# Performance work log

Measured on AMD Instinct MI355X. Metric: run time of the kernel, lower is better.

The kernel has to match this reference:

```python
import jax, jax.numpy as jnp
import numpy as np
from jax import lax

B, NQ, C = 2, 1024, 2048
H, DH = 16, 128
G, CD = 4, 512          # off_grps, off_dim = C // G
LR, HR = 24, 72         # low-res grid side, high-res grid side
INTER = 64
K = LR * LR             # sampled K/V tokens (grid_size == lr_size)


def setup_inputs() -> dict:
    key = jax.random.key(0)
    ks = jax.random.split(key, 16)
    s = 0.02
    d = {}
    d['hidden_states'] = jax.random.normal(ks[0], (B, NQ, C), jnp.float32)
    d['image_hd'] = jax.random.normal(ks[1], (B, HR * HR, C), jnp.float32)
    d['wq'] = jax.random.normal(ks[2], (C, C), jnp.float32) * s
    d['wk'] = jax.random.normal(ks[3], (C, C), jnp.float32) * s
    d['wv'] = jax.random.normal(ks[4], (C, C), jnp.float32) * s
    d['wo'] = jax.random.normal(ks[5], (C, C), jnp.float32) * s
    d['conv_dw_w'] = jax.random.normal(ks[6], (CD, 1, 3, 3), jnp.float32) * s
    d['ln1_w'] = jnp.ones((CD,), jnp.float32)
    d['ln1_b'] = jnp.zeros((CD,), jnp.float32)
    d['conv_lr_proj_w'] = jax.random.normal(ks[7], (INTER, CD), jnp.float32) * s
    d['proj_int_w'] = jax.random.normal(ks[8], (INTER, CD), jnp.float32) * s
    d['proj_int_b'] = jnp.zeros((INTER,), jnp.float32)
    d['ln2_w'] = jnp.ones((INTER,), jnp.float32)
    d['ln2_b'] = jnp.zeros((INTER,), jnp.float32)
    d['conv_off_w'] = jax.random.normal(ks[9], (2, INTER), jnp.float32) * s
    d['k_hd_w'] = jax.random.normal(ks[10], (C, C), jnp.float32) * s
    d['k_hd_b'] = jnp.zeros((C,), jnp.float32)
    d['v_hd_w'] = jax.random.normal(ks[11], (C, C), jnp.float32) * s
    d['v_hd_b'] = jnp.zeros((C,), jnp.float32)
    return d


def _ln_channels(x, w, b, eps=1e-5):
    # LayerNorm2d: normalize over channel axis of [N, C, H, W]
    mu = jnp.mean(x, axis=1, keepdims=True)
    var = jnp.var(x, axis=1, keepdims=True)
    xn = (x - mu) * lax.rsqrt(var + eps)
    return xn * w[None, :, None, None] + b[None, :, None, None]


def _tokens_to_grid(x, S):
    # [B, S*S, C] -> [B*G, CD, S, S]  (group channels like einops '(b) (h w) (g c) -> (b g) c h w')
    return x.reshape(B, S, S, G, CD).transpose(0, 3, 4, 1, 2).reshape(B * G, CD, S, S)


def _bilinear_sample(img, grid):
    # img [N, C, Hh, Wh]; grid [N, K, 2] (x, y) normalized to [-1, 1], align_corners=True
    N, Cc, Hh, Wh = img.shape
    x = (grid[..., 0] + 1.0) * 0.5 * (Wh - 1)
    y = (grid[..., 1] + 1.0) * 0.5 * (Hh - 1)
    x0f, y0f = jnp.floor(x), jnp.floor(y)
    wx = (x - x0f)[:, None, :]
    wy = (y - y0f)[:, None, :]
    x0 = jnp.clip(x0f.astype(jnp.int32), 0, Wh - 1)
    x1 = jnp.clip(x0 + 1, 0, Wh - 1)
    y0 = jnp.clip(y0f.astype(jnp.int32), 0, Hh - 1)
    y1 = jnp.clip(y0 + 1, 0, Hh - 1)
    imgf = img.reshape(N, Cc, Hh * Wh)
    gather = jax.vmap(lambda im, ix: im[:, ix])  # ([C,HW],[K]) -> [C,K]
    v00 = gather(imgf, y0 * Wh + x0)
    v01 = gather(imgf, y0 * Wh + x1)
    v10 = gather(imgf, y1 * Wh + x0)
    v11 = gather(imgf, y1 * Wh + x1)
    return (v00 * (1 - wx) * (1 - wy) + v01 * wx * (1 - wy)
            + v10 * (1 - wx) * wy + v11 * wx * wy)  # [N, C, K]


def _ref_grid():
    # normalized reference points as in _grid_generate (centers / (S-1) * 2 - 1)
    yy = (jnp.linspace(0.5, LR - 0.5, LR) / (LR - 1.0)) * 2.0 - 1.0
    xx = (jnp.linspace(0.5, LR - 0.5, LR) / (LR - 1.0)) * 2.0 - 1.0
    gy, gx = jnp.meshgrid(yy, xx, indexing='ij')
    return jnp.stack([gx, gy], axis=-1).reshape(K, 2)  # (x, y)


def reference(hidden_states, image_hd, wq, wk, wv, wo, conv_dw_w, ln1_w, ln1_b,
              conv_lr_proj_w, proj_int_w, proj_int_b, ln2_w, ln2_b, conv_off_w,
              k_hd_w, k_hd_b, v_hd_w, v_hd_b):
    # ---- QKV on the full sequence ----
    q = hidden_states @ wq.T
    k_txt = hidden_states @ wk.T
    v_txt = hidden_states @ wv.T

    # ---- offset network on LR image tokens (first LR*LR tokens) ----
    lr = _tokens_to_grid(hidden_states[:, :K, :], LR)          # [B*G, CD, LR, LR]
    x = lax.conv_general_dilated(lr, conv_dw_w, (1, 1), 'SAME',
                                 feature_group_count=CD,
                                 dimension_numbers=('NCHW', 'OIHW', 'NCHW'))
    x = jax.nn.silu(x)
    x = _ln_channels(x, ln1_w, ln1_b)
    x = jnp.einsum('nchw,oc->nohw', x, conv_lr_proj_w)          # 1x1 conv -> [B*G, INTER, LR, LR]
    # intention gate from spatially pooled group features
    pooled = jnp.mean(lr, axis=(2, 3))                          # [B*G, CD]
    gate = jax.nn.sigmoid(pooled @ proj_int_w.T + proj_int_b)   # [B*G, INTER]
    x = x * gate[:, :, None, None]
    x = _ln_channels(x, ln2_w, ln2_b)
    off = jnp.einsum('nchw,oc->nohw', x, conv_off_w)            # [B*G, 2, LR, LR]
    off = off.transpose(0, 2, 3, 1).reshape(B * G, K, 2)        # (x, y)
    pos = jnp.tanh(_ref_grid()[None] + off)                     # sampling locs in [-1, 1]

    # ---- deformable gather from HD features ----
    hd = _tokens_to_grid(image_hd, HR)                          # [B*G, CD, HR, HR]
    samp = _bilinear_sample(hd, pos)                            # [B*G, CD, K]
    samp = samp.reshape(B, G, CD, K).transpose(0, 3, 1, 2).reshape(B, K, C)
    k_hd = samp @ k_hd_w.T + k_hd_b
    v_hd = samp @ v_hd_w.T + v_hd_b

    # ---- attention: causal over text tokens, HD tokens fully visible ----
    k_all = jnp.concatenate([k_txt, k_hd], axis=1)              # [B, NQ+K, C]
    v_all = jnp.concatenate([v_txt, v_hd], axis=1)
    qh = q.reshape(B, NQ, H, DH).transpose(0, 2, 1, 3)
    kh = k_all.reshape(B, NQ + K, H, DH).transpose(0, 2, 1, 3)
    vh = v_all.reshape(B, NQ + K, H, DH).transpose(0, 2, 1, 3)
    scores = jnp.einsum('bhqd,bhkd->bhqk', qh, kh) / jnp.sqrt(jnp.float32(DH))
    col = jnp.arange(NQ + K)
    row = jnp.arange(NQ)
    allow = (col[None, :] >= NQ) | (col[None, :] <= row[:, None])
    scores = jnp.where(allow[None, None], scores, jnp.float32(-1e9))
    attn = jax.nn.softmax(scores, axis=-1)
    out = jnp.einsum('bhqk,bhkd->bhqd', attn, vh)
    out = out.transpose(0, 2, 1, 3).reshape(B, NQ, C)
    return out @ wo.T
```

## Files before the change

kernel.cpp:

```cpp
#include <hip/hip_runtime.h>

typedef unsigned short u16;
typedef unsigned int u32;
typedef __attribute__((ext_vector_type(8))) short bf8;
typedef __attribute__((ext_vector_type(4))) float f4;
typedef __attribute__((ext_vector_type(4))) unsigned short us4;

constexpr int B = 2;
constexpr int NQ = 1024;
constexpr int C = 2048;
constexpr int DH = 128;
constexpr int G = 4;
constexpr int CD = 512;
constexpr int LR = 24;
constexpr int HR = 72;
constexpr int INTER = 64;
constexpr int K = LR * LR;
constexpr int NKV = NQ + K;

#define MFMA16(a, b, c) __builtin_amdgcn_mfma_f32_16x16x32_bf16(a, b, c, 0, 0, 0)
#define GLDS(g, l)                                                         \
  __builtin_amdgcn_global_load_lds(                                        \
      (const __attribute__((address_space(1))) void*)(g),                  \
      (__attribute__((address_space(3))) void*)(l), 16, 0, 0)
#define SB()                               \
  do {                                     \
    __builtin_amdgcn_sched_barrier(0);     \
    __builtin_amdgcn_s_barrier();          \
    __builtin_amdgcn_sched_barrier(0);     \
  } while (0)
#define WVM(n)                                              \
  do {                                                      \
    asm volatile("s_waitcnt vmcnt(" #n ")" ::: "memory");   \
    __builtin_amdgcn_sched_barrier(0);                      \
  } while (0)

__device__ __forceinline__ u16 f2bf1(float f) {
  u32 u = __float_as_uint(f);
  u32 r = (u + 0x7fffu + ((u >> 16) & 1u)) >> 16;
  return (u16)r;
}

__global__ __launch_bounds__(256) void f2bf_k8v(
    const float* __restrict__ s0, const float* __restrict__ s1,
    const float* __restrict__ s2, const float* __restrict__ s3,
    const float* __restrict__ s4, const float* __restrict__ s5,
    const float* __restrict__ s6, const float* __restrict__ plrw,
    u16* __restrict__ d0, u16* __restrict__ d1, u16* __restrict__ d2,
    u16* __restrict__ d3, u16* __restrict__ d4, u16* __restrict__ d5,
    u16* __restrict__ d6, float* __restrict__ wt) {
  __shared__ u16 L[64 * 68];
  const int y = blockIdx.y;
  const int t = threadIdx.x;
  if (y == 7) {
    if (blockIdx.x >= 128) return;
    const int idx = blockIdx.x * 256 + t;
    wt[idx] = plrw[(idx & 63) * 512 + (idx >> 6)];
    return;
  }
  const float* s;
  u16* d;
  switch (y) {
    case 0: s = s0; d = d0; break;
    case 1: s = s1; d = d1; break;
    case 2: s = s2; d = d2; break;
    case 3: s = s3; d = d3; break;
    case 4: s = s4; d = d4; break;
    case 5: s = s5; d = d5; break;
    default: s = s6; d = d6; break;
  }
  const int pc = blockIdx.x;
  const int mb = pc >> 5, kb = pc & 31;
  const int rin = t >> 2, c0 = (t & 3) * 16;
  const float* src = s + (size_t)(mb * 64 + rin) * 2048 + kb * 64 + c0;
#pragma unroll
  for (int j = 0; j < 16; j += 4) {
    float4 v = *(const float4*)(src + j);
    L[rin * 68 + c0 + j] = f2bf1(v.x);
    L[rin * 68 + c0 + j + 1] = f2bf1(v.y);
    L[rin * 68 + c0 + j + 2] = f2bf1(v.z);
    L[rin * 68 + c0 + j + 3] = f2bf1(v.w);
  }
  __syncthreads();
  u16* dst = d + (size_t)pc * 4096 + t * 16;
#pragma unroll
  for (int gg = 0; gg < 2; ++gg) {
    const int g = t * 2 + gg;
    const int rh = g & 15, ks2 = (g >> 4) & 3, kc = (g >> 6) & 1, fr = g >> 7;
    const int row = fr * 16 + rh, cc = kc * 32 + ks2 * 8;
    us4 o0, o1;
    o0.x = L[row * 68 + cc];     o0.y = L[row * 68 + cc + 1];
    o0.z = L[row * 68 + cc + 2]; o0.w = L[row * 68 + cc + 3];
    o1.x = L[row * 68 + cc + 4]; o1.y = L[row * 68 + cc + 5];
    o1.z = L[row * 68 + cc + 6]; o1.w = L[row * 68 + cc + 7];
    *(us4*)(dst + gg * 8) = o0;
    *(us4*)(dst + gg * 8 + 4) = o1;
  }
}

__global__ __launch_bounds__(256) void dwpool16(const float* __restrict__ hs,
                                                const float* __restrict__ cdw,
                                                float* __restrict__ x1,
                                                float* __restrict__ pooled) {
  __shared__ float SH[16 * 577];
  const int bidx = blockIdx.x;
  const int n = bidx >> 5, cg = bidx & 31;
  const int b = n >> 2, g = n & 3;
  const int c0 = cg * 16;
  const int t = threadIdx.x;
  {
    const int c = t & 15, pr = t >> 4;
    const float* src = hs + (size_t)b * 1024 * 2048 + g * 512 + c0 + c;
#pragma unroll 4
    for (int j = 0; j < 36; ++j) {
      const int p = j * 16 + pr;
      SH[c * 577 + p] = src[(size_t)p * 2048];
    }
  }
  __syncthreads();
  {
    const int c = t >> 4, seg = t & 15;
    float s = 0.f;
    for (int i = 0; i < 36; ++i) s += SH[c * 577 + seg * 36 + i];
    s += __shfl_xor(s, 1);
    s += __shfl_xor(s, 2);
    s += __shfl_xor(s, 4);
    s += __shfl_xor(s, 8);
    if (seg == 0) pooled[n * 512 + c0 + c] = s * (1.f / 576.f);
  }
  const size_t base_out = (size_t)(n * 512 + c0) * 576;
  for (int j = 0; j < 36; ++j) {
    const int idx = j * 256 + t;
    const int c = idx / 576, p = idx - c * 576;
    const int yy0 = p / 24, xx0 = p - yy0 * 24;
    const float* wp = cdw + (c0 + c) * 9;
    float s = 0.f;
#pragma unroll
    for (int dy = -1; dy <= 1; ++dy)
#pragma unroll
      for (int dx = -1; dx <= 1; ++dx) {
        const int yy = yy0 + dy, xx = xx0 + dx;
        if (yy < 0 || yy >= 24 || xx < 0 || xx >= 24) continue;
        s += SH[c * 577 + yy * 24 + xx] * wp[(dy + 1) * 3 + dx + 1];
      }
    x1[base_out + idx] = s / (1.f + expf(-s));
  }
}

__global__ __launch_bounds__(512, 2) void gemm_queue(
    const u16* __restrict__ Ast, const u16* __restrict__ Wq,
    const u16* __restrict__ Wk, const u16* __restrict__ Wv,
    const u16* __restrict__ sampst, const u16* __restrict__ khwst,
    const u16* __restrict__ vhwst, const float* __restrict__ khb,
    const float* __restrict__ vhb, u16* __restrict__ outq,
    u16* __restrict__ kg, u16* __restrict__ vg, u32* __restrict__ qctr) {
  __shared__ u16 As[2][4][4096];
  __shared__ u16 Bs[2][4][4096];
  __shared__ int s_item;
  const int tid = threadIdx.x, lane = tid & 63, w = tid >> 6;
  const int ks = lane >> 4, r = lane & 15;

  while (true) {
    __syncthreads();
    if (tid == 0) s_item = (int)atomicAdd(qctr, 1u);
    __syncthreads();
    const int item = s_item;
    if (item >= 480) break;

    if (item < 192) {
      const int wm = w >> 2, wn = w & 3;
      const int swz = (item & 7) * 24 + (item >> 3);
      const int mt = swz / 24, nt = swz % 24;
      const u16* Wst = (nt < 8) ? Wq : (nt < 16) ? Wk : Wv;
      const int nb0 = (nt & 7) * 4;
      const int mb0 = mt * 4;

#define ST_A03(bi, kt)                                                        \
  do {                                                                        \
    GLDS(Ast + ((size_t)(mb0 + 0) * 32 + (kt)) * 4096 + tid * 8,              \
         &As[bi][0][tid * 8]);                                                \
    GLDS(Ast + ((size_t)(mb0 + 2) * 32 + (kt)) * 4096 + tid * 8,              \
         &As[bi][2][tid * 8]);                                                \
  } while (0)
#define ST_A47(bi, kt)                                                        \
  do {                                                                        \
    GLDS(Ast + ((size_t)(mb0 + 1) * 32 + (kt)) * 4096 + tid * 8,              \
         &As[bi][1][tid * 8]);                                                \
    GLDS(Ast + ((size_t)(mb0 + 3) * 32 + (kt)) * 4096 + tid * 8,              \
         &As[bi][3][tid * 8]);                                                \
  } while (0)
#define ST_B01(bi, kt)                                                        \
  do {                                                                        \
    GLDS(Wst + ((size_t)(nb0 + 0) * 32 + (kt)) * 4096 + tid * 8,              \
         &Bs[bi][0][tid * 8]);                                                \
    GLDS(Wst + ((size_t)(nb0 + 1) * 32 + (kt)) * 4096 + tid * 8,              \
         &Bs[bi][1][tid * 8]);                                                \
  } while (0)
#define ST_B23(bi, kt)                                                        \
  do {                                                                        \
    GLDS(Wst + ((size_t)(nb0 + 2) * 32 + (kt)) * 4096 + tid * 8,              \
         &Bs[bi][2][tid * 8]);                                                \
    GLDS(Wst + ((size_t)(nb0 + 3) * 32 + (kt)) * 4096 + tid * 8,              \
         &Bs[bi][3][tid * 8]);                                                \
  } while (0)
#define RD_A(dst, bi, half, kc)                                               \
  _Pragma("unroll") for (int i2 = 0; i2 < 4; ++i2) dst[i2] =                  \
      *(const bf8*)(&As[bi][wm * 2 + (half)]                                  \
                       [((i2 * 2 + (kc)) * 4 + ks) * 128 + r * 8]);
#define RD_B(dst, bi, kc)                                                     \
  _Pragma("unroll") for (int j2 = 0; j2 < 4; ++j2) dst[j2] =                  \
      *(const bf8*)(&Bs[bi][wn][((j2 * 2 + (kc)) * 4 + ks) * 128 + r * 8]);
#define MM(ACC, AF, BF)                                                       \
  do {                                                                        \
    __builtin_amdgcn_s_setprio(1);                                            \
    _Pragma("unroll") for (int i3 = 0; i3 < 4; ++i3)                          \
        _Pragma("unroll") for (int j3 = 0; j3 < 4; ++j3) ACC[i3][j3] =        \
            MFMA16(AF[i3], BF[j3], ACC[i3][j3]);                              \
    __builtin_amdgcn_s_setprio(0);                                            \
  } while (0)

      f4 accA[4][4], accB[4][4];
#pragma unroll
      for (int i = 0; i < 4; ++i)
#pragma unroll
        for (int j = 0; j < 4; ++j) {
          accA[i][j] = f4{0.f, 0.f, 0.f, 0.f};
          accB[i][j] = f4{0.f, 0.f, 0.f, 0.f};
        }
      bf8 af[4], b0[4], b1[4];

      ST_A03(0, 0); ST_B01(0, 0); ST_B23(0, 0); ST_A47(0, 0);
      ST_A03(1, 1); ST_B01(1, 1);
      WVM(6);
      SB();

      for (int t = 0; t < 32; ++t) {
        const int buf = t & 1;
        RD_A(af, buf, 0, 0);
        RD_B(b0, buf, 0);
        if (t + 1 < 32) ST_B23(buf ^ 1, t + 1);
        SB();
        MM(accA, af, b0);
        SB();
        RD_A(af, buf, 0, 1);
        RD_B(b1, buf, 1);
        if (t + 1 < 32) ST_A47(buf ^ 1, t + 1);
        SB();
        MM(accA, af, b1);
        if (t + 1 < 32) { WVM(8); } else { WVM(0); }
        SB();
        RD_A(af, buf, 1, 0);
        if (t + 2 < 32) ST_A03(buf, t + 2);
        SB();
        MM(accB, af, b0);
        SB();
        RD_A(af, buf, 1, 1);
        if (t + 2 < 32) ST_B01(buf, t + 2);
        SB();
        MM(accB, af, b1);
        if (t + 2 < 32) { WVM(6); } else if (t + 1 < 32) { WVM(2); }
        SB();
      }

#define EPI(ACC, HALF)                                                        \
  _Pragma("unroll") for (int i = 0; i < 4; ++i)                               \
      _Pragma("unroll") for (int j = 0; j < 4; ++j)                           \
          _Pragma("unroll") for (int rr = 0; rr < 4; ++rr) {                  \
    const int m = mt * 256 + wm * 128 + (HALF)*64 + i * 16 + ks * 4 + rr;     \
    const int n = nt * 256 + wn * 64 + j * 16 + r;                            \
    const float v = ACC[i][j][rr];                                            \
    const int sel = n >> 11, nn = n & 2047, hh = nn >> 7, dd = nn & 127;      \
    const int bb = m >> 10, qq = m & 1023;                                    \
    const u16 bv = f2bf1(v);                                                  \
    if (sel == 0) {                                                           \
      outq[(size_t)m * 2048 + nn] = bv;                                       \
    } else if (sel == 1) {                                                    \
      kg[(((size_t)(bb * 16 + hh) * 50 + (qq >> 5)) * 16 + (dd >> 3)) * 256 + \
         (qq & 31) * 8 + (dd & 7)] = bv;                                      \
    } else {                                                                  \
      vg[((size_t)(bb * 16 + hh) * 200 + (qq >> 3)) * 1024 + dd * 8 +         \
         (qq & 7)] = bv;                                                      \
    }                                                                         \
  }
      EPI(accA, 0)
      EPI(accB, 1)
#undef EPI
    } else {
      u16* A3 = &As[0][0][0];
      u16* B3 = &Bs[0][0][0];
      const int htile = item - 192;
      const bool is_v = (htile >= 144);
      const int hb = is_v ? (htile - 144) : htile;
      const int mt = hb / 16, nt = hb % 16;
      const int ma0 = mt * 2, nb0 = nt * 2;
      const int wr = w >> 2, wc = w & 3;
      const u16* Wsrc = is_v ? vhwst : khwst;

#define HDS1(bi, kt)                                                          \
  do {                                                                        \
    const int kb_ = (kt) >> 1, kc_ = (kt) & 1;                                \
    GLDS(sampst + ((size_t)(ma0 + (w >> 2)) * 32 + kb_) * 4096 +              \
             (w & 3) * 1024 + kc_ * 512 + lane * 8,                           \
         &A3[(bi)*4096 + w * 512 + lane * 8]);                                \
    GLDS(Wsrc + ((size_t)(nb0 + (w >> 2)) * 32 + kb_) * 4096 +                \
             (w & 3) * 1024 + kc_ * 512 + lane * 8,                           \
         &B3[(bi)*4096 + w * 512 + lane * 8]);                                \
  } while (0)

      f4 acc[4][2];
#pragma unroll
      for (int i = 0; i < 4; ++i)
#pragma unroll
        for (int j = 0; j < 2; ++j) acc[i][j] = f4{0.f, 0.f, 0.f, 0.f};

      HDS1(0, 0);
      HDS1(1, 1);
      int rd = 0;
      for (int kt = 0; kt < 64; ++kt) {
        SB();
        if (kt + 2 < 64) {
          const int wb = (rd + 2 >= 3) ? rd - 1 : rd + 2;
          HDS1(wb, kt + 2);
          WVM(4);
        } else if (kt + 1 < 64) {
          WVM(2);
        } else {
          WVM(0);
        }
        SB();
        bf8 af2[4], bw[2];
#pragma unroll
        for (int i = 0; i < 4; ++i)
          af2[i] = *(const bf8*)(&A3[rd * 4096 + (wr * 4 + i) * 512 +
                                     ks * 128 + r * 8]);
#pragma unroll
        for (int j = 0; j < 2; ++j)
          bw[j] = *(const bf8*)(&B3[rd * 4096 + (wc * 2 + j) * 512 +
                                    ks * 128 + r * 8]);
        __builtin_amdgcn_s_setprio(1);
#pragma unroll
        for (int i = 0; i < 4; ++i)
#pragma unroll
          for (int j = 0; j < 2; ++j)
            acc[i][j] = MFMA16(af2[i], bw[j], acc[i][j]);
        __builtin_amdgcn_s_setprio(0);
        rd = (rd + 1 >= 3) ? 0 : rd + 1;
      }
#undef HDS1
      const int rbase = ks * 4;
      const float* bias = is_v ? vhb : khb;
#pragma unroll
      for (int i = 0; i < 4; ++i)
#pragma unroll
        for (int j = 0; j < 2; ++j) {
          const int nn = nt * 128 + (wc * 2 + j) * 16 + r;
          const int hh = nn >> 7, dd = nn & 127;
#pragma unroll
          for (int rr = 0; rr < 4; ++rr) {
            const int m = mt * 128 + wr * 64 + i * 16 + rbase + rr;
            const int bb = m / 576;
            const int kv = 1024 + (m - bb * 576);
            const u16 bv = f2bf1(acc[i][j][rr] + bias[nn]);
            if (!is_v) {
              kg[(((size_t)(bb * 16 + hh) * 50 + (kv >> 5)) * 16 + (dd >> 3)) *
                     256 +
                 (kv & 31) * 8 + (dd & 7)] = bv;
            } else {
              vg[((size_t)(bb * 16 + hh) * 200 + (kv >> 3)) * 1024 + dd * 8 +
                 (kv & 7)] = bv;
            }
          }
        }
    }
  }
}

__global__ __launch_bounds__(256) void gemm_out3(const u16* __restrict__ Ast,
                                                 const u16* __restrict__ W0,
                                                 float* __restrict__ outf) {
  __shared__ u16 As[3][4096];
  __shared__ u16 Bs[3][4096];
  const int tid = threadIdx.x, lane = tid & 63, w = tid >> 6;
  const int wr = w >> 1, wc = w & 1;
  const int ksl = lane >> 4, rl = lane & 15;
  const int xcd = blockIdx.x & 7, idx = blockIdx.x >> 3;
  const int mt = (xcd >> 2) * 8 + idx / 4;
  const int nt = (xcd & 3) * 4 + idx % 4;
  const u16* Wp = W0;
  const int ma0 = mt * 2;
  const int nb0 = nt * 2;

#define GST2(dstArr, srcBase, tb0, kt)                                     \
  do {                                                                     \
    const int kb_ = (kt) >> 1, kc_ = (kt) & 1;                             \
    _Pragma("unroll") for (int r2 = 0; r2 < 2; ++r2) {                     \
      const int run = r2 * 4 + w;                                          \
      GLDS(srcBase + ((size_t)((tb0) + (run >> 2)) * 32 + kb_) * 4096 +    \
               (run & 3) * 1024 + kc_ * 512 + lane * 8,                    \
           &dstArr[run * 512 + lane * 8]);                                 \
    }                                                                      \
  } while (0)

  f4 acc[4][4];
#pragma unroll
  for (int i = 0; i < 4; ++i)
#pragma unroll
    for (int j = 0; j < 4; ++j) acc[i][j] = f4{0.f, 0.f, 0.f, 0.f};

  GST2(As[0], Ast, ma0, 0);
  GST2(Bs[0], Wp, nb0, 0);
  GST2(As[1], Ast, ma0, 1);
  GST2(Bs[1], Wp, nb0, 1);
  int rd = 0;
  for (int kt = 0; kt < 64; ++kt) {
    SB();
    if (kt + 2 < 64) {
      const int wb = (rd + 2 >= 3) ? rd - 1 : rd + 2;
      GST2(As[wb], Ast, ma0, kt + 2);
      GST2(Bs[wb], Wp, nb0, kt + 2);
      WVM(8);
    } else if (kt + 1 < 64) {
      WVM(4);
    } else {
      WVM(0);
    }
    SB();
    bf8 af[4], bw[4];
#pragma unroll
    for (int i = 0; i < 4; ++i)
      af[i] = *(const bf8*)(&As[rd][(wr * 4 + i) * 512 + ksl * 128 + rl * 8]);
#pragma unroll
    for (int j = 0; j < 4; ++j)
      bw[j] = *(const bf8*)(&Bs[rd][(wc * 4 + j) * 512 + ksl * 128 + rl * 8]);
    __builtin_amdgcn_s_setprio(1);
#pragma unroll
    for (int i = 0; i < 4; ++i)
#pragma unroll
      for (int j = 0; j < 4; ++j)
        acc[i][j] = MFMA16(af[i], bw[j], acc[i][j]);
    __builtin_amdgcn_s_setprio(0);
    rd = (rd + 1 >= 3) ? 0 : rd + 1;
  }
#undef GST2

  const int rbase = ksl * 4;
#pragma unroll
  for (int i = 0; i < 4; ++i)
#pragma unroll
    for (int j = 0; j < 4; ++j) {
      const int n = nt * 128 + wc * 64 + j * 16 + rl;
#pragma unroll
      for (int rr = 0; rr < 4; ++rr) {
        const int m = mt * 128 + wr * 64 + i * 16 + rbase + rr;
        outf[(size_t)m * 2048 + n] = acc[i][j][rr];
      }
    }
}

__global__ __launch_bounds__(256) void lnproj_gate(
    const float* __restrict__ x1, const float* __restrict__ ln1w,
    const float* __restrict__ ln1b, const float* __restrict__ wt,
    const float* __restrict__ pooled, const float* __restrict__ piw,
    const float* __restrict__ pib, float* __restrict__ x2,
    float* __restrict__ gate) {
  __shared__ float Xs[512][68];
  __shared__ float rs[4][64], rss[4][64];
  const int bidx = blockIdx.x;
  const int t = threadIdx.x;
  if (bidx >= 72) {
    const int idx = (bidx - 72) * 256 + t;
    const int n = idx >> 6, o = idx & 63;
    const float* pb = pooled + n * 512;
    const float* wb = piw + o * 512;
    float s = pib[o];
    for (int c = 0; c < 512; ++c) s += pb[c] * wb[c];
    gate[idx] = 1.f / (1.f + expf(-s));
    return;
  }
  const int n = bidx / 9, pc = bidx % 9;
  const int p0 = pc * 64;
  {
    const int pl = t & 63, c4 = t >> 6;
    const float* src = x1 + (size_t)n * 512 * 576 + p0 + pl;
#pragma unroll 4
    for (int j = 0; j < 128; ++j) {
      const int c = j * 4 + c4;
      Xs[c][pl] = src[(size_t)c * 576];
    }
  }
  __syncthreads();
  {
    const int pl = t & 63, q = t >> 6;
    float s = 0.f, ss = 0.f;
    for (int c = q * 128; c < q * 128 + 128; ++c) {
      const float v = Xs[c][pl];
      s += v;
      ss += v * v;
    }
    rs[q][pl] = s;
    rss[q][pl] = ss;
    __syncthreads();
    const float S = rs[0][pl] + rs[1][pl] + rs[2][pl] + rs[3][pl];
    const float SS = rss[0][pl] + rss[1][pl] + rss[2][pl] + rss[3][pl];
    const float mean = S * (1.f / 512.f);
    const float inv = rsqrtf(SS * (1.f / 512.f) - mean * mean + 1e-5f);
    for (int c = q * 128; c < q * 128 + 128; ++c)
      Xs[c][pl] = (Xs[c][pl] - mean) * inv * ln1w[c] + ln1b[c];
  }
  __syncthreads();
  {
    const int o4 = (t & 15) * 4, pl0 = (t >> 4) * 4;
    float acc[4][4] = {};
    for (int c = 0; c < 512; ++c) {
      const f4 xv = *(const f4*)(&Xs[c][pl0]);
      const f4 wv = *(const f4*)(&wt[c * 64 + o4]);
#pragma unroll
      for (int i = 0; i < 4; ++i)
#pragma unroll
        for (int j = 0; j < 4; ++j) acc[i][j] += wv[i] * xv[j];
    }
#pragma unroll
    for (int i = 0; i < 4; ++i) {
      f4 ov;
      ov[0] = acc[i][0]; ov[1] = acc[i][1];
      ov[2] = acc[i][2]; ov[3] = acc[i][3];
      *(f4*)(&x2[(size_t)(n * 64 + o4 + i) * 576 + p0 + pl0]) = ov;
    }
  }
}

__global__ __launch_bounds__(256) void pos_sample(
    const float* __restrict__ x2, const float* __restrict__ gate,
    const float* __restrict__ ln2w, const float* __restrict__ ln2b,
    const float* __restrict__ offw, const float* __restrict__ img,
    u16* __restrict__ sampst) {
  const int bk = blockIdx.x;
  const int b = bk / K, k = bk % K;
  __shared__ int s_idx[G][4];
  __shared__ float s_w[G][4];
  const int t = threadIdx.x;
  const int g = t >> 6, lane = t & 63;
  {
    const int n = b * G + g;
    float v = x2[((size_t)n * INTER + lane) * K + k] * gate[n * INTER + lane];
    float s = v, ss = v * v;
    for (int o = 32; o; o >>= 1) {
      s += __shfl_xor(s, o);
      ss += __shfl_xor(ss, o);
    }
    const float mean = s * (1.f / INTER);
    const float var = ss * (1.f / INTER) - mean * mean;
    const float xn = (v - mean) * rsqrtf(var + 1e-5f) * ln2w[lane] + ln2b[lane];
    float ox = xn * offw[lane];
    float oy = xn * offw[INTER + lane];
    for (int o = 32; o; o >>= 1) {
      ox += __shfl_xor(ox, o);
      oy += __shfl_xor(oy, o);
    }
    if (lane == 0) {
      const int yi = k / LR, xi = k % LR;
      const float rx = (xi + 0.5f) / 23.f * 2.f - 1.f;
      const float ry = (yi + 0.5f) / 23.f * 2.f - 1.f;
      const float px = tanhf(rx + ox), py = tanhf(ry + oy);
      const float x = (px + 1.f) * 0.5f * (HR - 1);
      const float y = (py + 1.f) * 0.5f * (HR - 1);
      const float x0f = floorf(x), y0f = floorf(y);
      const float wx = x - x0f, wy = y - y0f;
      const int x0 = min(max((int)x0f, 0), HR - 1);
      const int x1 = min(x0 + 1, HR - 1);
      const int y0 = min(max((int)y0f, 0), HR - 1);
      const int y1 = min(y0 + 1, HR - 1);
      s_idx[g][0] = y0 * HR + x0;
      s_idx[g][1] = y0 * HR + x1;
      s_idx[g][2] = y1 * HR + x0;
      s_idx[g][3] = y1 * HR + x1;
      s_w[g][0] = (1.f - wx) * (1.f - wy);
      s_w[g][1] = wx * (1.f - wy);
      s_w[g][2] = (1.f - wx) * wy;
      s_w[g][3] = wx * wy;
    }
  }
  __syncthreads();
  const int m = b * 576 + k;
  const int mb = m >> 6, fr = (m >> 4) & 3, r = m & 15;
  const int ch0 = t * 8;
  const int gg = ch0 >> 9;
  const float* ib = img + (size_t)b * HR * HR * C + ch0;
  float v[8];
#pragma unroll
  for (int j = 0; j < 8; ++j) v[j] = 0.f;
#pragma unroll
  for (int q = 0; q < 4; ++q) {
    const float wq_ = s_w[gg][q];
    const float* p = ib + (size_t)s_idx[gg][q] * C;
    const float4 a = *(const float4*)p;
    const float4 c = *(const float4*)(p + 4);
    v[0] += wq_ * a.x; v[1] += wq_ * a.y; v[2] += wq_ * a.z; v[3] += wq_ * a.w;
    v[4] += wq_ * c.x; v[5] += wq_ * c.y; v[6] += wq_ * c.z; v[7] += wq_ * c.w;
  }
  const int kb = ch0 >> 6, kc = (ch0 >> 5) & 1, ks3 = (ch0 >> 3) & 3;
  u16* dst = sampst + ((size_t)(mb * 32 + kb)) * 4096 +
             (((fr * 2 + kc) * 4 + ks3) * 16 + r) * 8;
  us4 o0, o1;
  o0.x = f2bf1(v[0]); o0.y = f2bf1(v[1]); o0.z = f2bf1(v[2]); o0.w = f2bf1(v[3]);
  o1.x = f2bf1(v[4]); o1.y = f2bf1(v[5]); o1.z = f2bf1(v[6]); o1.w = f2bf1(v[7]);
  *(us4*)dst = o0;
  *(us4*)(dst + 4) = o1;
}

__global__ __launch_bounds__(256) void attn_u64(
    const u16* __restrict__ qb, const u16* __restrict__ kg,
    const u16* __restrict__ vg, u16* __restrict__ aob_st) {
  const int i = blockIdx.x;
  const int pair = i & 255, half = i >> 8;
  const int bh = pair & 31;
  const int q8 = pair >> 5;
  const int qblk = half ? (15 - q8) : q8;
  const int b = bh >> 4, h = bh & 15;
  const int q0 = qblk * 64;
  const int tid = threadIdx.x, lane = tid & 63, w = tid >> 6;
  const int qw = q0 + w * 16;
  const int col = lane & 15, kpart = lane >> 4, rbase = kpart * 4;
  __shared__ u16 Ks[2][8192];
  __shared__ u16 Vs[2][8192];
  __shared__ u16 Pl[4][16 * 72];
  bf8 qf[4];
  {
    const u16* qp =
        qb + (size_t)(b * 1024 + qw + col) * 2048 + h * 128 + kpart * 8;
#pragma unroll
    for (int dc = 0; dc < 4; ++dc) qf[dc] = *(const bf8*)(qp + dc * 32);
  }
  f4 o[8];
#pragma unroll
  for (int df = 0; df < 8; ++df) o[df] = f4{0.f, 0.f, 0.f, 0.f};
  float m_r[4] = {-1e30f, -1e30f, -1e30f, -1e30f};
  float l_p[4] = {0.f, 0.f, 0.f, 0.f};
  const float scale = 0.08838834764831845f;
  const int nt_text = qblk + 1;
  const int nt = nt_text + 9;
  const u16* kbh = kg + (size_t)bh * (NKV * 128);
  const u16* vbh = vg + (size_t)bh * (NKV * 128);
  u16* pw = &Pl[w][0];

#define ASTG64(bi, kv0)                                                       \
  do {                                                                        \
    const u16* gk = kbh + (size_t)((kv0) >> 5) * 4096 + w * 2048 + lane * 8;  \
    GLDS(gk, &Ks[bi][w * 2048 + lane * 8]);                                   \
    GLDS(gk + 512, &Ks[bi][w * 2048 + 512 + lane * 8]);                       \
    GLDS(gk + 1024, &Ks[bi][w * 2048 + 1024 + lane * 8]);                     \
    GLDS(gk + 1536, &Ks[bi][w * 2048 + 1536 + lane * 8]);                     \
    const u16* gv = vbh + (size_t)((kv0) >> 3) * 1024 + w * 2048 + lane * 8;  \
    GLDS(gv, &Vs[bi][w * 2048 + lane * 8]);                                   \
    GLDS(gv + 512, &Vs[bi][w * 2048 + 512 + lane * 8]);                       \
    GLDS(gv + 1024, &Vs[bi][w * 2048 + 1024 + lane * 8]);                     \
    GLDS(gv + 1536, &Vs[bi][w * 2048 + 1536 + lane * 8]);                     \
  } while (0)

  ASTG64(0, 0);
  int cur = 0;
  for (int t = 0; t < nt; ++t) {
    const bool is_text = t < nt_text;
    const int kv0 = is_text ? (t << 6) : (1024 + ((t - nt_text) << 6));
    SB();
    if (t + 1 < nt) {
      const int t1 = t + 1;
      const int kv1 =
          (t1 < nt_text) ? (t1 << 6) : (1024 + ((t1 - nt_text) << 6));
      ASTG64(cur ^ 1, kv1);
      WVM(8);
    } else {
      WVM(0);
    }
    SB();
    const u16* ksb = &Ks[cur][0];
    const u16* vsb = &Vs[cur][0];
    f4 s0 = {0.f, 0.f, 0.f, 0.f}, s1 = {0.f, 0.f, 0.f, 0.f};
    f4 s2 = {0.f, 0.f, 0.f, 0.f}, s3 = {0.f, 0.f, 0.f, 0.f};
    __builtin_amdgcn_s_setprio(1);
#pragma unroll
    for (int dc = 0; dc < 4; ++dc) {
      const int dblk = dc * 4 + kpart;
      bf8 k0f = *(const bf8*)(ksb + (dblk * 32 + col) * 8);
      bf8 k1f = *(const bf8*)(ksb + (dblk * 32 + 16 + col) * 8);
      bf8 k2f = *(const bf8*)(ksb + 4096 + (dblk * 32 + col) * 8);
      bf8 k3f = *(const bf8*)(ksb + 4096 + (dblk * 32 + 16 + col) * 8);
      s0 = MFMA16(qf[dc], k0f, s0);
      s1 = MFMA16(qf[dc], k1f, s1);
      s2 = MFMA16(qf[dc], k2f, s2);
      s3 = MFMA16(qf[dc], k3f, s3);
    }
    __builtin_amdgcn_s_setprio(0);
    float sa[4][4], loc[4], p[4][4];
    bool grow = false;
    const bool need_mask = is_text && (kv0 + 63 > qw);
#pragma unroll
    for (int rr = 0; rr < 4; ++rr) {
      float a0 = s0[rr] * scale, a1 = s1[rr] * scale;
      float a2 = s2[rr] * scale, a3 = s3[rr] * scale;
      if (need_mask) {
        const int qg = qw + rbase + rr;
        if (kv0 + col > qg) a0 = -1e30f;
        if (kv0 + 16 + col > qg) a1 = -1e30f;
        if (kv0 + 32 + col > qg) a2 = -1e30f;
        if (kv0 + 48 + col > qg) a3 = -1e30f;
      }
      sa[rr][0] = a0; sa[rr][1] = a1; sa[rr][2] = a2; sa[rr][3] = a3;
      loc[rr] = fmaxf(fmaxf(a0, a1), fmaxf(a2, a3));
      grow |= (loc[rr] > m_r[rr] + 8.f);
    }
    if (__any(grow)) {
      float fr[4];
#pragma unroll
      for (int rr = 0; rr < 4; ++rr) {
        float mx = loc[rr];
        mx = fmaxf(mx, __shfl_xor(mx, 1));
        mx = fmaxf(mx, __shfl_xor(mx, 2));
        mx = fmaxf(mx, __shfl_xor(mx, 4));
        mx = fmaxf(mx, __shfl_xor(mx, 8));
        const float mn = fmaxf(m_r[rr], mx);
        fr[rr] = __expf(m_r[rr] - mn);
        m_r[rr] = mn;
#pragma unroll
        for (int jj = 0; jj < 4; ++jj) p[rr][jj] = __expf(sa[rr][jj] - mn);
        l_p[rr] = l_p[rr] * fr[rr] + p[rr][0] + p[rr][1] + p[rr][2] + p[rr][3];
      }
#pragma unroll
      for (int df = 0; df < 8; ++df) {
        o[df][0] *= fr[0]; o[df][1] *= fr[1];
        o[df][2] *= fr[2]; o[df][3] *= fr[3];
      }
    } else {
#pragma unroll
      for (int rr = 0; rr < 4; ++rr) {
#pragma unroll
        for (int jj = 0; jj < 4; ++jj) p[rr][jj] = __expf(sa[rr][jj] - m_r[rr]);
        l_p[rr] += p[rr][0] + p[rr][1] + p[rr][2] + p[rr][3];
      }
    }
#pragma unroll
    for (int rr = 0; rr < 4; ++rr) {
      pw[(rbase + rr) * 72 + col] = f2bf1(p[rr][0]);
      pw[(rbase + rr) * 72 + 16 + col] = f2bf1(p[rr][1]);
      pw[(rbase + rr) * 72 + 32 + col] = f2bf1(p[rr][2]);
      pw[(rbase + rr) * 72 + 48 + col] = f2bf1(p[rr][3]);
    }
    bf8 pa0 = *(const bf8*)(pw + col * 72 + kpart * 8);
    bf8 pa1 = *(const bf8*)(pw + col * 72 + 32 + kpart * 8);
    __builtin_amdgcn_s_setprio(1);
#pragma unroll
    for (int df = 0; df < 8; ++df) {
      bf8 vf0 = *(const bf8*)(vsb + (kpart * 128 + df * 16 + col) * 8);
      bf8 vf1 = *(const bf8*)(vsb + ((kpart + 4) * 128 + df * 16 + col) * 8);
      o[df] = MFMA16(pa0, vf0, o[df]);
      o[df] = MFMA16(pa1, vf1, o[df]);
    }
    __builtin_amdgcn_s_setprio(0);
    cur ^= 1;
  }
#undef ASTG64
  float inv[4];
#pragma unroll
  for (int rr = 0; rr < 4; ++rr) {
    float ps = l_p[rr];
    ps += __shfl_xor(ps, 1);
    ps += __shfl_xor(ps, 2);
    ps += __shfl_xor(ps, 4);
    ps += __shfl_xor(ps, 8);
    inv[rr] = 1.f / ps;
  }
#pragma unroll
  for (int rr = 0; rr < 4; ++rr) {
    const int m = b * 1024 + qw + rbase + rr;
    const int mb = m >> 6, fr3 = (m >> 4) & 3, r16 = m & 15;
#pragma unroll
    for (int df = 0; df < 8; ++df) {
      const int ncol = h * 128 + df * 16 + col;
      const int kb = ncol >> 6, kc = (ncol >> 5) & 1, ks3 = (ncol >> 3) & 3,
                j0 = ncol & 7;
      aob_st[((size_t)(mb * 32 + kb)) * 4096 +
             (((fr3 * 2 + kc) * 4 + ks3) * 16 + r16) * 8 + j0] =
          f2bf1(o[df][rr] * inv[rr]);
    }
  }
}

extern "C" void kernel_launch(void* const* d_in, const int* in_sizes, int n_in,
                              void* d_out, int out_size, void* d_ws,
                              size_t ws_size, hipStream_t stream) {
  const float* hs = (const float*)d_in[0];
  const float* img = (const float*)d_in[1];
  const float* wq = (const float*)d_in[2];
  const float* wk = (const float*)d_in[3];
  const float* wv = (const float*)d_in[4];
  const float* wo = (const float*)d_in[5];
  const float* cdw = (const float*)d_in[6];
  const float* ln1w = (const float*)d_in[7];
  const float* ln1b = (const float*)d_in[8];
  const float* plrw = (const float*)d_in[9];
  const float* piw = (const float*)d_in[10];
  const float* pib = (const float*)d_in[11];
  const float* ln2w = (const float*)d_in[12];
  const float* ln2b = (const float*)d_in[13];
  const float* offw = (const float*)d_in[14];
  const float* khw = (const float*)d_in[15];
  const float* khb = (const float*)d_in[16];
  const float* vhw = (const float*)d_in[17];
  const float* vhb = (const float*)d_in[18];
  float* outp = (float*)d_out;

  u16* wsp = (u16*)d_ws;
  const size_t SZ = 4194304;
  u16* hs_st = wsp;
  u16* wq_st = wsp + SZ;
  u16* wk_st = wsp + 2 * SZ;
  u16* wv_st = wsp + 3 * SZ;
  u16* wo_st = wsp + 4 * SZ;
  u16* khw_st = wsp + 5 * SZ;
  u16* vhw_st = wsp + 6 * SZ;
  u16* qb_bf = wsp + 7 * SZ;
  u16* samp_st = wsp + 8 * SZ;
  u16* kg = wsp + 8 * SZ + 2359296;
  u16* vg = kg + 6553600;
  float* x1b = (float*)kg + 2359296;
  float* x2b = x1b + 2359296;
  float* poolb = x2b + 294912;
  float* gb = poolb + 4096;
  float* wtb = (float*)(vg + 6553600);
  u32* qctr = (u32*)(wtb + 32768);
  u16* aob_st = wq_st;

  dim3 blk(256);
  dwpool16<<<dim3(256), blk, 0, stream>>>(hs, cdw, x1b, poolb);
  f2bf_k8v<<<dim3(1024, 8), blk, 0, stream>>>(hs, wq, wk, wv, wo, khw, vhw,
                                              plrw, hs_st, wq_st, wk_st,
                                              wv_st, wo_st, khw_st, vhw_st,
                                              wtb);
  lnproj_gate<<<dim3(74), blk, 0, stream>>>(x1b, ln1w, ln1b, wtb, poolb, piw,
                                            pib, x2b, gb);
  pos_sample<<<dim3(B * K), blk, 0, stream>>>(x2b, gb, ln2w, ln2b, offw, img,
                                              samp_st);
  hipMemsetAsync(qctr, 0, 4, stream);
  gemm_queue<<<dim3(256), dim3(512), 0, stream>>>(
      hs_st, wq_st, wk_st, wv_st, samp_st, khw_st, vhw_st, khb, vhb, qb_bf,
      kg, vg, qctr);
  attn_u64<<<dim3(512), blk, 0, stream>>>(qb_bf, kg, vg, aob_st);
  gemm_out3<<<dim3(256), blk, 0, stream>>>(aob_st, wo_st, outp);
}
```

Before: 320.0 us.

## Fuse wo fp32-to-bf16 conversion into output GEMM B-tile loading

Drops the separate pre-conversion of wo to a staged bf16 layout in the conversion kernel. The output GEMM now reads wo as fp32 from global memory into registers, converts it to bf16 and writes it to LDS inside its pipelined K loop, with a register prefetch one step ahead. This removes one 16 MB fp32 read plus 8 MB bf16 write-and-reread pass. In exchange the GEMM moves twice the bytes for B, does conversion ALU work and LDS stores per tile, and waits on vmcnt(0) each iteration, which weakens its async pipelining.

```diff
diff --git a/kernel.cpp b/kernel.cpp
--- a/kernel.cpp
+++ b/kernel.cpp
@@ -34,6 +34,11 @@
     asm volatile("s_waitcnt vmcnt(" #n ")" ::: "memory");   \
     __builtin_amdgcn_sched_barrier(0);                      \
   } while (0)
+#define LGKM0()                                             \
+  do {                                                      \
+    asm volatile("s_waitcnt lgkmcnt(0)" ::: "memory");      \
+    __builtin_amdgcn_sched_barrier(0);                      \
+  } while (0)
 
 __device__ __forceinline__ u16 f2bf1(float f) {
   u32 u = __float_as_uint(f);
@@ -45,14 +50,13 @@
     const float* __restrict__ s0, const float* __restrict__ s1,
     const float* __restrict__ s2, const float* __restrict__ s3,
     const float* __restrict__ s4, const float* __restrict__ s5,
-    const float* __restrict__ s6, const float* __restrict__ plrw,
-    u16* __restrict__ d0, u16* __restrict__ d1, u16* __restrict__ d2,
-    u16* __restrict__ d3, u16* __restrict__ d4, u16* __restrict__ d5,
-    u16* __restrict__ d6, float* __restrict__ wt) {
+    const float* __restrict__ plrw, u16* __restrict__ d0,
+    u16* __restrict__ d1, u16* __restrict__ d2, u16* __restrict__ d3,
+    u16* __restrict__ d4, u16* __restrict__ d5, float* __restrict__ wt) {
   __shared__ u16 L[64 * 68];
   const int y = blockIdx.y;
   const int t = threadIdx.x;
-  if (y == 7) {
+  if (y == 6) {
     if (blockIdx.x >= 128) return;
     const int idx = blockIdx.x * 256 + t;
     wt[idx] = plrw[(idx & 63) * 512 + (idx >> 6)];
@@ -66,8 +70,7 @@
     case 2: s = s2; d = d2; break;
     case 3: s = s3; d = d3; break;
     case 4: s = s4; d = d4; break;
-    case 5: s = s5; d = d5; break;
-    default: s = s6; d = d6; break;
+    default: s = s5; d = d5; break;
   }
   const int pc = blockIdx.x;
   const int mb = pc >> 5, kb = pc & 31;
@@ -376,7 +379,7 @@
 }
 
 __global__ __launch_bounds__(256) void gemm_out3(const u16* __restrict__ Ast,
-                                                 const u16* __restrict__ W0,
+                                                 const float* __restrict__ woF,
                                                  float* __restrict__ outf) {
   __shared__ u16 As[3][4096];
   __shared__ u16 Bs[3][4096];
@@ -386,44 +389,76 @@
   const int xcd = blockIdx.x & 7, idx = blockIdx.x >> 3;
   const int mt = (xcd >> 2) * 8 + idx / 4;
   const int nt = (xcd & 3) * 4 + idx % 4;
-  const u16* Wp = W0;
   const int ma0 = mt * 2;
   const int nb0 = nt * 2;
 
-#define GST2(dstArr, srcBase, tb0, kt)                                     \
+#define GST2A(dstArr, tb0, kt)                                             \
   do {                                                                     \
     const int kb_ = (kt) >> 1, kc_ = (kt) & 1;                             \
     _Pragma("unroll") for (int r2 = 0; r2 < 2; ++r2) {                     \
       const int run = r2 * 4 + w;                                          \
-      GLDS(srcBase + ((size_t)((tb0) + (run >> 2)) * 32 + kb_) * 4096 +    \
+      GLDS(Ast + ((size_t)((tb0) + (run >> 2)) * 32 + kb_) * 4096 +        \
                (run & 3) * 1024 + kc_ * 512 + lane * 8,                    \
            &dstArr[run * 512 + lane * 8]);                                 \
     }                                                                      \
   } while (0)
 
+  const float* woA = woF + (size_t)((nb0 + 0) * 64 + w * 16 + rl) * 2048 + ksl * 8;
+  const float* woB = woF + (size_t)((nb0 + 1) * 64 + w * 16 + rl) * 2048 + ksl * 8;
+  float4 b0r, b1r, b2r, b3r;
+#define BLOAD(kt)                                        \
+  do {                                                   \
+    b0r = *(const float4*)(woA + (kt) * 32);             \
+    b1r = *(const float4*)(woA + (kt) * 32 + 4);         \
+    b2r = *(const float4*)(woB + (kt) * 32);             \
+    b3r = *(const float4*)(woB + (kt) * 32 + 4);         \
+  } while (0)
+#define BWRITE(wb)                                                          \
+  do {                                                                      \
+    us4 q;                                                                  \
+    q.x = f2bf1(b0r.x); q.y = f2bf1(b0r.y);                                 \
+    q.z = f2bf1(b0r.z); q.w = f2bf1(b0r.w);                                 \
+    *(us4*)(&Bs[wb][w * 512 + lane * 8]) = q;                               \
+    q.x = f2bf1(b1r.x); q.y = f2bf1(b1r.y);                                 \
+    q.z = f2bf1(b1r.z); q.w = f2bf1(b1r.w);                                 \
+    *(us4*)(&Bs[wb][w * 512 + lane * 8 + 4]) = q;                           \
+    q.x = f2bf1(b2r.x); q.y = f2bf1(b2r.y);                                 \
+    q.z = f2bf1(b2r.z); q.w = f2bf1(b2r.w);                                 \
+    *(us4*)(&Bs[wb][(4 + w) * 512 + lane * 8]) = q;                         \
+    q.x = f2bf1(b3r.x); q.y = f2bf1(b3r.y);                                 \
+    q.z = f2bf1(b3r.z); q.w = f2bf1(b3r.w);                                 \
+    *(us4*)(&Bs[wb][(4 + w) * 512 + lane * 8 + 4]) = q;                     \
+  } while (0)
+
   f4 acc[4][4];
 #pragma unroll
   for (int i = 0; i < 4; ++i)
 #pragma unroll
     for (int j = 0; j < 4; ++j) acc[i][j] = f4{0.f, 0.f, 0.f, 0.f};
 
-  GST2(As[0], Ast, ma0, 0);
-  GST2(Bs[0], Wp, nb0, 0);
-  GST2(As[1], Ast, ma0, 1);
-  GST2(Bs[1], Wp, nb0, 1);
+  GST2A(As[0], ma0, 0);
+  GST2A(As[1], ma0, 1);
+  BLOAD(0);
+  WVM(0);
+  BWRITE(0);
+  BLOAD(1);
+  WVM(0);
+  BWRITE(1);
+  BLOAD(2);
+  LGKM0();
   int rd = 0;
   for (int kt = 0; kt < 64; ++kt) {
     SB();
     if (kt + 2 < 64) {
       const int wb = (rd + 2 >= 3) ? rd - 1 : rd + 2;
-      GST2(As[wb], Ast, ma0, kt + 2);
-      GST2(Bs[wb], Wp, nb0, kt + 2);
-      WVM(8);
-    } else if (kt + 1 < 64) {
-      WVM(4);
+      WVM(0);
+      BWRITE(wb);
+      GST2A(As[wb], ma0, kt + 2);
+      if (kt + 3 < 64) BLOAD(kt + 3);
     } else {
       WVM(0);
     }
+    LGKM0();
     SB();
     bf8 af[4], bw[4];
 #pragma unroll
@@ -441,7 +476,9 @@
     __builtin_amdgcn_s_setprio(0);
     rd = (rd + 1 >= 3) ? 0 : rd + 1;
   }
-#undef GST2
+#undef GST2A
+#undef BLOAD
+#undef BWRITE
 
   const int rbase = ksl * 4;
 #pragma unroll
@@ -815,7 +852,6 @@
   u16* wq_st = wsp + SZ;
   u16* wk_st = wsp + 2 * SZ;
   u16* wv_st = wsp + 3 * SZ;
-  u16* wo_st = wsp + 4 * SZ;
   u16* khw_st = wsp + 5 * SZ;
   u16* vhw_st = wsp + 6 * SZ;
   u16* qb_bf = wsp + 7 * SZ;
@@ -832,10 +868,9 @@
 
   dim3 blk(256);
   dwpool16<<<dim3(256), blk, 0, stream>>>(hs, cdw, x1b, poolb);
-  f2bf_k8v<<<dim3(1024, 8), blk, 0, stream>>>(hs, wq, wk, wv, wo, khw, vhw,
-                                              plrw, hs_st, wq_st, wk_st,
-                                              wv_st, wo_st, khw_st, vhw_st,
-                                              wtb);
+  f2bf_k8v<<<dim3(1024, 7), blk, 0, stream>>>(hs, wq, wk, wv, khw, vhw, plrw,
+                                              hs_st, wq_st, wk_st, wv_st,
+                                              khw_st, vhw_st, wtb);
   lnproj_gate<<<dim3(74), blk, 0, stream>>>(x1b, ln1w, ln1b, wtb, poolb, piw,
                                             pib, x2b, gb);
   pos_sample<<<dim3(B * K), blk, 0, stream>>>(x2b, gb, ln2w, ln2b, offw, img,
@@ -845,5 +880,5 @@
       hs_st, wq_st, wk_st, wv_st, samp_st, khw_st, vhw_st, khb, vhb, qb_bf,
       kg, vg, qctr);
   attn_u64<<<dim3(512), blk, 0, stream>>>(qb_bf, kg, vg, aob_st);
-  gemm_out3<<<dim3(256), blk, 0, stream>>>(aob_st, wo_st, outp);
+  gemm_out3<<<dim3(256), blk, 0, stream>>>(aob_st, wo, outp);
 }
```

Result: slower. 350.9 us (+9.7%).
